# Kernel optimization log

Hardware: AMD Instinct MI355X
Metric: run time of the kernel (lower is better)

## Reference

```python
import jax, jax.numpy as jnp
import numpy as np

HID = 1024   # hidden_size
HEADS = 16   # multi_head
DH = 64      # hidden_size_head
FF = 4096    # ff_size
EPS = 1e-6   # LayerNorm epsilon
NEG = -1e9


def setup_inputs() -> dict:
    key = jax.random.key(0)
    ks = jax.random.split(key, 24)
    B, LI, LQ, LK = 16, 512, 64, 128
    s = 0.02

    def w(k, shape):
        return jax.random.normal(k, shape, jnp.float32) * s

    return {
        "img_feat": jax.random.normal(ks[0], (B, LI, HID), jnp.float32),
        "ques": jax.random.normal(ks[1], (B, LQ, HID), jnp.float32),
        "kg": jax.random.normal(ks[2], (B, LK, HID), jnp.float32),
        "ques_mask": jax.random.randint(ks[3], (B, LQ), 0, 2, jnp.int32),
        "kg_mask": jax.random.randint(ks[4], (B, LK), 0, 2, jnp.int32),
        # stacked params for the 3 MHAtt blocks; torch Linear weight layout [out, in]
        "att_qw": w(ks[5], (3, HID, HID)), "att_qb": jnp.zeros((3, HID), jnp.float32),
        "att_kw": w(ks[6], (3, HID, HID)), "att_kb": jnp.zeros((3, HID), jnp.float32),
        "att_vw": w(ks[7], (3, HID, HID)), "att_vb": jnp.zeros((3, HID), jnp.float32),
        "att_ow": w(ks[8], (3, HID, HID)), "att_ob": jnp.zeros((3, HID), jnp.float32),
        "ffn_w1": w(ks[9], (FF, HID)), "ffn_b1": jnp.zeros((FF,), jnp.float32),
        "ffn_w2": w(ks[10], (HID, FF)), "ffn_b2": jnp.zeros((HID,), jnp.float32),
        "ln_g": jnp.ones((4, HID), jnp.float32), "ln_b": jnp.zeros((4, HID), jnp.float32),
    }


def _ln(x, g, b):
    m = jnp.mean(x, axis=-1, keepdims=True)
    v = jnp.mean(jnp.square(x - m), axis=-1, keepdims=True)
    return g * (x - m) / jnp.sqrt(v + EPS) + b


def _mha(v_in, k_in, q_in, mask, qw, qb, kw, kb, vw, vb, ow, ob):
    B = q_in.shape[0]

    def proj(x, wt, bi):  # [B,S,H] -> [B,heads,S,DH]
        y = jnp.einsum('bsh,oh->bso', x, wt) + bi
        return y.reshape(B, -1, HEADS, DH).transpose(0, 2, 1, 3)

    q = proj(q_in, qw, qb)
    k = proj(k_in, kw, kb)
    v = proj(v_in, vw, vb)
    scores = jnp.einsum('bhqd,bhkd->bhqk', q, k) / jnp.sqrt(jnp.float32(DH))
    if mask is not None:
        scores = jnp.where(mask[:, None, None, :] == 1, NEG, scores)
    a = jax.nn.softmax(scores, axis=-1)  # dropout is identity at eval
    o = jnp.einsum('bhqk,bhkd->bhqd', a, v).transpose(0, 2, 1, 3).reshape(B, -1, HID)
    return jnp.einsum('bsh,oh->bso', o, ow) + ob


def reference(img_feat, ques, kg, ques_mask, kg_mask,
              att_qw, att_qb, att_kw, att_kb, att_vw, att_vb, att_ow, att_ob,
              ffn_w1, ffn_b1, ffn_w2, ffn_b2, ln_g, ln_b):
    x = img_feat
    # self-attention on image features (no mask)
    x = _ln(x + _mha(x, x, x, None,
                     att_qw[0], att_qb[0], att_kw[0], att_kb[0],
                     att_vw[0], att_vb[0], att_ow[0], att_ob[0]), ln_g[0], ln_b[0])
    # cross-attention to question
    x = _ln(x + _mha(ques, ques, x, ques_mask,
                     att_qw[1], att_qb[1], att_kw[1], att_kb[1],
                     att_vw[1], att_vb[1], att_ow[1], att_ob[1]), ln_g[1], ln_b[1])
    # cross-attention to knowledge graph facts
    x = _ln(x + _mha(kg, kg, x, kg_mask,
                     att_qw[2], att_qb[2], att_kw[2], att_kb[2],
                     att_vw[2], att_vb[2], att_ow[2], att_ob[2]), ln_g[2], ln_b[2])
    # FFN: Linear -> ReLU -> Linear (dropout identity at eval)
    h = jax.nn.relu(jnp.einsum('bsh,fh->bsf', x, ffn_w1) + ffn_b1)
    f = jnp.einsum('bsf,hf->bsh', h, ffn_w2) + ffn_b2
    x = _ln(x + f, ln_g[3], ln_b[3])
    return x
```

## Files before the change

kernel.cpp:

```cpp
#include <hip/hip_runtime.h>
#include <math.h>

#define HIDN 1024
#define NHEADS 16
#define DHEAD 64
#define FFD 4096
#define LN_EPS 1e-6f
#define NEGV -1e9f

typedef __bf16 bf16_t;
typedef __bf16 bf16x8 __attribute__((ext_vector_type(8)));
typedef float f32x4 __attribute__((ext_vector_type(4)));
typedef unsigned short ushort8 __attribute__((ext_vector_type(8)));
typedef unsigned short ushort4v __attribute__((ext_vector_type(4)));

__device__ __forceinline__ unsigned short f2bf(float f) {
    unsigned u = __float_as_uint(f);
    return (unsigned short)((u + 0x7FFFu + ((u >> 16) & 1u)) >> 16);
}
__device__ __forceinline__ float bf2f(unsigned short u) {
    return __uint_as_float((unsigned)u << 16);
}
__device__ __forceinline__ void gld16(const void* g, void* l) {
    __builtin_amdgcn_global_load_lds(
        (const __attribute__((address_space(1))) void*)g,
        (__attribute__((address_space(3))) void*)l, 16, 0, 0);
}

template<int RELU>
__global__ __launch_bounds__(256)
void gemm_mfma(const bf16_t* __restrict__ A, const bf16_t* __restrict__ W,
               const float* __restrict__ ba, const float* __restrict__ bb,
               const float* __restrict__ bc, const float* __restrict__ bd,
               unsigned short* __restrict__ Cb, int M, int N, int K)
{
    __shared__ __align__(16) bf16_t As[2][128 * 64];
    __shared__ __align__(16) bf16_t Bs[2][128 * 64];

    const int tid  = threadIdx.x;
    const int wid  = tid >> 6;
    const int lane = tid & 63;
    const int m0 = blockIdx.x * 128;
    const int n0 = blockIdx.y * 128;
    const int wm = (wid & 1) * 64;
    const int wn = (wid >> 1) * 64;

    const int sr = (wid << 3) + (lane >> 3);
    const int sk = (((lane & 7) ^ (lane >> 3)) * 8);
    const bf16_t* pa = A + (size_t)(m0 + sr) * K + sk;
    const bf16_t* pb = W + (size_t)(n0 + sr) * K + sk;
    const int lofs = (wid << 3) * 64;

    const int lr  = lane & 15;
    const int hi_ = lane >> 4;
    const int ch0 = ((hi_ + 0) ^ (lane & 7)) * 8;
    const int ch1 = ((hi_ + 4) ^ (lane & 7)) * 8;

    f32x4 acc[4][4];
    #pragma unroll
    for (int i = 0; i < 4; ++i)
        #pragma unroll
        for (int j = 0; j < 4; ++j) acc[i][j] = (f32x4){0.f, 0.f, 0.f, 0.f};

    auto stage = [&](int buf, int koff) {
        #pragma unroll
        for (int c = 0; c < 4; ++c) {
            gld16(pa + (size_t)c * 32 * K + koff, &As[buf][lofs + c * 32 * 64]);
            gld16(pb + (size_t)c * 32 * K + koff, &Bs[buf][lofs + c * 32 * 64]);
        }
    };
    auto compute = [&](int buf) {
        const bf16_t* fa = &As[buf][(wm + lr) * 64];
        const bf16_t* fb = &Bs[buf][(wn + lr) * 64];
        #pragma unroll
        for (int kk = 0; kk < 2; ++kk) {
            const int ch = kk ? ch1 : ch0;
            bf16x8 a[4], b[4];
            #pragma unroll
            for (int i = 0; i < 4; ++i) {
                a[i] = *(const bf16x8*)(fa + i * 16 * 64 + ch);
                b[i] = *(const bf16x8*)(fb + i * 16 * 64 + ch);
            }
            #pragma unroll
            for (int i = 0; i < 4; ++i)
                #pragma unroll
                for (int j = 0; j < 4; ++j)
                    acc[i][j] = __builtin_amdgcn_mfma_f32_16x16x32_bf16(
                        a[i], b[j], acc[i][j], 0, 0, 0);
        }
    };

    stage(0, 0);
    asm volatile("s_waitcnt vmcnt(0)" ::: "memory");
    __syncthreads();

    for (int k0 = 0; k0 < K; k0 += 128) {
        if (k0 + 64 < K) stage(1, k0 + 64);
        compute(0);
        asm volatile("s_waitcnt vmcnt(0)" ::: "memory");
        __syncthreads();
        if (k0 + 128 < K) stage(0, k0 + 128);
        compute(1);
        asm volatile("s_waitcnt vmcnt(0)" ::: "memory");
        __syncthreads();
    }

    const int seg = n0 >> 10;
    const float* bias = (seg == 0) ? ba : (seg == 1) ? bb : (seg == 2) ? bc : bd;
    const int nl = (n0 & 1023);
    const int er = wm + (lane >> 4) * 4;
    const int ec = wn + (lane & 15);
    float bv[4];
    #pragma unroll
    for (int j = 0; j < 4; ++j) bv[j] = bias[nl + ec + j * 16];
    #pragma unroll
    for (int i = 0; i < 4; ++i)
        #pragma unroll
        for (int j = 0; j < 4; ++j)
            #pragma unroll
            for (int r = 0; r < 4; ++r) {
                float v = acc[i][j][r] + bv[j];
                if (RELU) v = fmaxf(v, 0.f);
                Cb[(size_t)(m0 + er + i * 16 + r) * N + (n0 + ec + j * 16)] = f2bf(v);
            }
}

template<int RELU>
__global__ __launch_bounds__(512, 1)
void gemm_mfma256(const bf16_t* __restrict__ A, const bf16_t* __restrict__ W,
                  const float* __restrict__ ba, const float* __restrict__ bb,
                  const float* __restrict__ bc, const float* __restrict__ bd,
                  unsigned short* __restrict__ Cb, int M, int N, int K)
{
    __shared__ __align__(16) bf16_t As[2][256 * 64];
    __shared__ __align__(16) bf16_t Bs[2][256 * 64];

    const int tid  = threadIdx.x;
    const int wid  = tid >> 6;
    const int lane = tid & 63;
    const int lo   = lane & 15;
    const int hi   = lane >> 4;

    const int GY = gridDim.y;
    const int id = blockIdx.y * gridDim.x + blockIdx.x;
    const int xcd = id & 7;
    const int c   = id >> 3;
    const int CN  = GY >> 1;
    const int m_idx = ((xcd & 3) << 3) + (c & 7);
    const int n_idx = (xcd >> 2) * CN + (c >> 3);
    const int m0 = m_idx * 256;
    const int n0 = n_idx * 256;

    const int wm = (wid & 1) * 128;
    const int wn = (wid >> 1) * 64;

    const int srow = tid >> 3;
    const int ssk  = (((tid & 7) ^ (srow & 7)) * 8);
    const bf16_t* pa = A + (size_t)(m0 + srow) * K + ssk;
    const bf16_t* pb = W + (size_t)(n0 + srow) * K + ssk;
    const int lbase = (wid << 3) * 64;

    auto stage = [&](int buf, int koff) {
        #pragma unroll
        for (int i = 0; i < 4; ++i) {
            gld16(pa + (size_t)i * 64 * K + koff, &As[buf][i * 64 * 64 + lbase]);
            gld16(pb + (size_t)i * 64 * K + koff, &Bs[buf][i * 64 * 64 + lbase]);
        }
    };

    f32x4 acc[8][4];
    #pragma unroll
    for (int f = 0; f < 8; ++f)
        #pragma unroll
        for (int g = 0; g < 4; ++g) acc[f][g] = (f32x4){0.f, 0.f, 0.f, 0.f};

    auto compute = [&](int buf) {
        #pragma unroll
        for (int kk = 0; kk < 2; ++kk) {
            bf16x8 a[8], b[4];
            #pragma unroll
            for (int f = 0; f < 8; ++f) {
                const int row = wm + f * 16 + lo;
                const int ch  = ((kk * 4 + hi) ^ (lo & 7)) * 8;
                a[f] = *(const bf16x8*)&As[buf][row * 64 + ch];
            }
            #pragma unroll
            for (int g = 0; g < 4; ++g) {
                const int row = wn + g * 16 + lo;
                const int ch  = ((kk * 4 + hi) ^ (lo & 7)) * 8;
                b[g] = *(const bf16x8*)&Bs[buf][row * 64 + ch];
            }
            #pragma unroll
            for (int f = 0; f < 8; ++f)
                #pragma unroll
                for (int g = 0; g < 4; ++g)
                    acc[f][g] = __builtin_amdgcn_mfma_f32_16x16x32_bf16(
                        a[f], b[g], acc[f][g], 0, 0, 0);
        }
    };

    stage(0, 0);
    asm volatile("s_waitcnt vmcnt(0)" ::: "memory");
    __syncthreads();

    for (int k0 = 0; k0 < K; k0 += 128) {
        if (k0 + 64 < K) stage(1, k0 + 64);
        compute(0);
        asm volatile("s_waitcnt vmcnt(0)" ::: "memory");
        __syncthreads();
        if (k0 + 128 < K) stage(0, k0 + 128);
        compute(1);
        asm volatile("s_waitcnt vmcnt(0)" ::: "memory");
        __syncthreads();
    }

    const int seg = n0 >> 10;
    const float* bias = (seg == 0) ? ba : (seg == 1) ? bb : (seg == 2) ? bc : bd;
    const int nl = (n0 & 1023);
    float bv[4];
    #pragma unroll
    for (int g = 0; g < 4; ++g) bv[g] = bias[nl + wn + g * 16 + lo];
    #pragma unroll
    for (int f = 0; f < 8; ++f)
        #pragma unroll
        for (int g = 0; g < 4; ++g)
            #pragma unroll
            for (int r = 0; r < 4; ++r) {
                float v = acc[f][g][r] + bv[g];
                if (RELU) v = fmaxf(v, 0.f);
                Cb[(size_t)(m0 + wm + f * 16 + hi * 4 + r) * N
                   + (n0 + wn + g * 16 + lo)] = f2bf(v);
            }
}

template<int HAS_MASK>
__global__ __launch_bounds__(512, 2)
void attn_mfma(const bf16_t* __restrict__ Q, const bf16_t* __restrict__ K,
               const bf16_t* __restrict__ V, int qstride, int kvstride,
               const int* __restrict__ mask,
               unsigned short* __restrict__ O, int Lk)
{
    __shared__ __align__(16) unsigned short Ks[64][72];
    __shared__ __align__(16) unsigned short Vt[64][72];
    __shared__ __align__(16) unsigned short Ps[128][72];
    __shared__ int smask[64];

    const int tid  = threadIdx.x;
    const int wid  = tid >> 6;
    const int lane = tid & 63;
    const int lo   = lane & 15;
    const int hi   = lane >> 4;
    const int h    = blockIdx.x;
    const int b    = blockIdx.y;
    const int Lq   = 512;

    bf16x8 qf[4][2];
    #pragma unroll
    for (int s4 = 0; s4 < 4; ++s4) {
        const bf16_t* qp = Q + (size_t)(b*Lq + s4*128 + wid*16 + lo) * qstride
                             + h*DHEAD + hi*8;
        qf[s4][0] = *(const bf16x8*)qp;
        qf[s4][1] = *(const bf16x8*)(qp + 32);
    }

    float mrun[4][4], lrun[4][4];
    f32x4 Oc[4][4];
    #pragma unroll
    for (int s4 = 0; s4 < 4; ++s4)
        #pragma unroll
        for (int r = 0; r < 4; ++r) {
            mrun[s4][r] = -INFINITY; lrun[s4][r] = 0.f;
            Oc[s4][r] = (f32x4){0.f, 0.f, 0.f, 0.f};
        }

    ushort8 r0, r1;
    int mreg = 0;

    auto load_tile = [&](int k0) {
        if (tid < 256) {
            const int sr = tid >> 2, sc = (tid & 3) * 16;
            const unsigned short* kp = (const unsigned short*)
                (K + (size_t)(b*Lk + k0 + sr) * kvstride + h*DHEAD + sc);
            r0 = *(const ushort8*)kp;
            r1 = *(const ushort8*)(kp + 8);
        } else {
            const int t2 = tid - 256, sr = t2 >> 2, sc = (t2 & 3) * 16;
            const unsigned short* vp = (const unsigned short*)
                (V + (size_t)(b*Lk + k0 + sr) * kvstride + h*DHEAD + sc);
            r0 = *(const ushort8*)vp;
            r1 = *(const ushort8*)(vp + 8);
        }
        if (HAS_MASK && tid < 64) mreg = mask[b*Lk + k0 + tid];
    };
    auto store_tile = [&]() {
        if (tid < 256) {
            const int sr = tid >> 2, sc = (tid & 3) * 16;
            const int x = ((sr >> 3) & 7) << 3;
            *(ushort8*)&Ks[sr][sc ^ x]       = r0;
            *(ushort8*)&Ks[sr][(sc + 8) ^ x] = r1;
        } else {
            const int t2 = tid - 256, sr = t2 >> 2, sc = (t2 & 3) * 16;
            #pragma unroll
            for (int t = 0; t < 8; ++t) {
                const int d0 = sc + t, d1 = sc + 8 + t;
                Vt[d0][sr ^ (((d0 >> 3) & 7) << 3)] = r0[t];
                Vt[d1][sr ^ (((d1 >> 3) & 7) << 3)] = r1[t];
            }
        }
        if (HAS_MASK && tid < 64) smask[tid] = mreg;
    };

    load_tile(0);
    store_tile();
    __syncthreads();

    int k0 = 0;
    while (true) {
        const bool more = (k0 + 64 < Lk);
        if (more) load_tile(k0 + 64);

        #pragma unroll
        for (int s4 = 0; s4 < 4; ++s4) {
            f32x4 sv[4];
            #pragma unroll
            for (int j = 0; j < 4; ++j) sv[j] = (f32x4){0.f, 0.f, 0.f, 0.f};
            #pragma unroll
            for (int kk = 0; kk < 2; ++kk) {
                #pragma unroll
                for (int j = 0; j < 4; ++j) {
                    const int krow = j*16 + lo;
                    const int kcol = (kk*32 + hi*8) ^ (((krow >> 3) & 7) << 3);
                    bf16x8 bfrag = *(const bf16x8*)&Ks[krow][kcol];
                    sv[j] = __builtin_amdgcn_mfma_f32_16x16x32_bf16(
                        qf[s4][kk], bfrag, sv[j], 0, 0, 0);
                }
            }
            #pragma unroll
            for (int j = 0; j < 4; ++j) {
                bool msk = HAS_MASK ? (smask[j*16 + lo] != 0) : false;
                #pragma unroll
                for (int r = 0; r < 4; ++r) {
                    float x = sv[j][r] * 0.125f;
                    sv[j][r] = msk ? NEGV : x;
                }
            }
            #pragma unroll
            for (int r = 0; r < 4; ++r) {
                float tm = fmaxf(fmaxf(sv[0][r], sv[1][r]), fmaxf(sv[2][r], sv[3][r]));
                #pragma unroll
                for (int m = 1; m < 16; m <<= 1) tm = fmaxf(tm, __shfl_xor(tm, m));
                float mnew = fmaxf(mrun[s4][r], tm);
                float f = __expf(mrun[s4][r] - mnew);
                float ps = 0.f;
                #pragma unroll
                for (int j = 0; j < 4; ++j) {
                    float p = __expf(sv[j][r] - mnew);
                    sv[j][r] = p;
                    ps += p;
                }
                #pragma unroll
                for (int m = 1; m < 16; m <<= 1) ps += __shfl_xor(ps, m);
                lrun[s4][r] = lrun[s4][r] * f + ps;
                mrun[s4][r] = mnew;
                #pragma unroll
                for (int n = 0; n < 4; ++n) Oc[s4][n][r] *= f;
                #pragma unroll
                for (int j = 0; j < 4; ++j)
                    Ps[wid*16 + hi*4 + r][j*16 + lo] = f2bf(sv[j][r]);
            }
            #pragma unroll
            for (int kk = 0; kk < 2; ++kk) {
                bf16x8 pa = *(const bf16x8*)&Ps[wid*16 + lo][kk*32 + hi*8];
                #pragma unroll
                for (int n = 0; n < 4; ++n) {
                    const int vrow = n*16 + lo;
                    const int vcol = (kk*32 + hi*8) ^ (((vrow >> 3) & 7) << 3);
                    bf16x8 vf = *(const bf16x8*)&Vt[vrow][vcol];
                    Oc[s4][n] = __builtin_amdgcn_mfma_f32_16x16x32_bf16(
                        pa, vf, Oc[s4][n], 0, 0, 0);
                }
            }
        }

        if (!more) break;
        __syncthreads();
        store_tile();
        __syncthreads();
        k0 += 64;
    }

    #pragma unroll
    for (int s4 = 0; s4 < 4; ++s4)
        #pragma unroll
        for (int r = 0; r < 4; ++r) {
            float inv = 1.f / lrun[s4][r];
            const size_t row = (size_t)(b*Lq + s4*128 + wid*16 + hi*4 + r) * HIDN
                             + h*DHEAD;
            #pragma unroll
            for (int n = 0; n < 4; ++n)
                O[row + n*16 + lo] = f2bf(Oc[s4][n][r] * inv);
        }
}

template<int WF32, int WBF>
__global__ __launch_bounds__(256)
void ln_res_b(const unsigned short* __restrict__ X, const unsigned short* __restrict__ R,
              const float* __restrict__ G, const float* __restrict__ Bv,
              unsigned short* __restrict__ OutB, float* __restrict__ OutF)
{
    const int row = blockIdx.x;
    const int tid = threadIdx.x;
    const size_t base = (size_t)row * HIDN + tid * 4;
    ushort4v xv = *(const ushort4v*)(X + base);
    ushort4v rv = *(const ushort4v*)(R + base);
    float y[4];
    #pragma unroll
    for (int t = 0; t < 4; ++t) y[t] = bf2f(xv[t]) + bf2f(rv[t]);
    float s1 = y[0] + y[1] + y[2] + y[3];
    float s2 = y[0]*y[0] + y[1]*y[1] + y[2]*y[2] + y[3]*y[3];
    #pragma unroll
    for (int m = 1; m < 64; m <<= 1) {
        s1 += __shfl_xor(s1, m);
        s2 += __shfl_xor(s2, m);
    }
    __shared__ float red1[4], red2[4];
    const int wave = tid >> 6, lane = tid & 63;
    if (lane == 0) { red1[wave] = s1; red2[wave] = s2; }
    __syncthreads();
    s1 = red1[0] + red1[1] + red1[2] + red1[3];
    s2 = red2[0] + red2[1] + red2[2] + red2[3];
    const float mean = s1 * (1.f / HIDN);
    const float var  = s2 * (1.f / HIDN) - mean * mean;
    const float inv  = rsqrtf(var + LN_EPS);
    float4 gv = *(const float4*)(G + tid*4);
    float4 bv = *(const float4*)(Bv + tid*4);
    float o[4];
    o[0] = gv.x * (y[0]-mean) * inv + bv.x;
    o[1] = gv.y * (y[1]-mean) * inv + bv.y;
    o[2] = gv.z * (y[2]-mean) * inv + bv.z;
    o[3] = gv.w * (y[3]-mean) * inv + bv.w;
    if (WBF) {
        ushort4v ob;
        #pragma unroll
        for (int t = 0; t < 4; ++t) ob[t] = f2bf(o[t]);
        *(ushort4v*)(OutB + base) = ob;
    }
    if (WF32) {
        float4 of = {o[0], o[1], o[2], o[3]};
        *(float4*)(OutF + base) = of;
    }
}

struct CvtArgs {
    const float* src[32];
    unsigned short* dst[32];
};

__global__ __launch_bounds__(256)
void cvt_units(CvtArgs args)
{
    const float* s = args.src[blockIdx.y];
    unsigned short* d = args.dst[blockIdx.y];
    const int i = blockIdx.x * 256 + threadIdx.x;
    const float4* p = (const float4*)s + (size_t)i * 2;
    float4 a = p[0], b = p[1];
    ushort8 o;
    o[0] = f2bf(a.x); o[1] = f2bf(a.y); o[2] = f2bf(a.z); o[3] = f2bf(a.w);
    o[4] = f2bf(b.x); o[5] = f2bf(b.y); o[6] = f2bf(b.z); o[7] = f2bf(b.w);
    ((ushort8*)d)[i] = o;
}

extern "C" void kernel_launch(void* const* d_in, const int* in_sizes, int n_in,
                              void* d_out, int out_size, void* d_ws, size_t ws_size,
                              hipStream_t stream)
{
    const float* img   = (const float*)d_in[0];
    const float* ques  = (const float*)d_in[1];
    const float* kg    = (const float*)d_in[2];
    const int*   qmask = (const int*)d_in[3];
    const int*   kmask = (const int*)d_in[4];
    const float* qw = (const float*)d_in[5];
    const float* qb = (const float*)d_in[6];
    const float* kw = (const float*)d_in[7];
    const float* kb = (const float*)d_in[8];
    const float* vw = (const float*)d_in[9];
    const float* vb = (const float*)d_in[10];
    const float* ow = (const float*)d_in[11];
    const float* ob = (const float*)d_in[12];
    const float* w1 = (const float*)d_in[13];
    const float* b1 = (const float*)d_in[14];
    const float* w2 = (const float*)d_in[15];
    const float* b2 = (const float*)d_in[16];
    const float* lng = (const float*)d_in[17];
    const float* lnb = (const float*)d_in[18];
    float* out = (float*)d_out;

    const int B = 16;
    const int NX = B * 512;
    const size_t WSTEP = (size_t)1024 * 1024;
    const size_t MB = (size_t)1 << 20;
    const size_t MELEM = (size_t)1024 * 1024;

    char* wsb = (char*)d_ws;
    unsigned short* xb    = (unsigned short*)(wsb);
    unsigned short* bM    = (unsigned short*)(wsb + 16*MB);
    unsigned short* bOb   = (unsigned short*)(wsb + 32*MB);
    unsigned short* quesb = (unsigned short*)(wsb + 48*MB);
    unsigned short* kgb   = (unsigned short*)(wsb + 50*MB);
    unsigned short* wa    = (unsigned short*)(wsb + 56*MB);
    unsigned short* bQKV  = (unsigned short*)(wsb + 96*MB);
    unsigned short* bKV   = (unsigned short*)(wsb + 144*MB);
    unsigned short* hb    = (unsigned short*)(wsb + 96*MB);

    CvtArgs ca;
    int u = 0;
    auto addu = [&](const float* src, int melems, unsigned short* dst) {
        for (int i = 0; i < melems; ++i) {
            ca.src[u] = src + (size_t)i * MELEM;
            ca.dst[u] = dst + (size_t)i * MELEM;
            ++u;
        }
    };
    addu(qw + 0*WSTEP, 1, wa + 0*MELEM);
    addu(kw + 0*WSTEP, 1, wa + 1*MELEM);
    addu(vw + 0*WSTEP, 1, wa + 2*MELEM);
    addu(qw + 1*WSTEP, 1, wa + 3*MELEM);
    addu(kw + 1*WSTEP, 1, wa + 4*MELEM);
    addu(vw + 1*WSTEP, 1, wa + 5*MELEM);
    addu(qw + 2*WSTEP, 1, wa + 6*MELEM);
    addu(kw + 2*WSTEP, 1, wa + 7*MELEM);
    addu(vw + 2*WSTEP, 1, wa + 8*MELEM);
    addu(ow + 0*WSTEP, 1, wa + 9*MELEM);
    addu(ow + 1*WSTEP, 1, wa + 10*MELEM);
    addu(ow + 2*WSTEP, 1, wa + 11*MELEM);
    addu(w1, 4, wa + 12*MELEM);
    addu(w2, 4, wa + 16*MELEM);
    addu(img,  8, xb);
    addu(ques, 1, quesb);
    addu(kg,   2, kgb);

    dim3 blk(256);
    cvt_units<<<dim3(512, u), blk, 0, stream>>>(ca);

    auto gemm = [&](const unsigned short* A, const unsigned short* W,
                    const float* ba, const float* bb_, const float* bc, const float* bd,
                    unsigned short* C, int M, int N, int K, int relu) {
        if (N >= 3072 && (M % 256) == 0 && (N % 256) == 0
            && ((M / 256) % 8) == 0 && ((N / 256) % 2) == 0 && (K % 128) == 0) {
            dim3 grid(M / 256, N / 256);
            if (relu) gemm_mfma256<1><<<grid, dim3(512), 0, stream>>>(
                (const bf16_t*)A, (const bf16_t*)W, ba, bb_, bc, bd, C, M, N, K);
            else      gemm_mfma256<0><<<grid, dim3(512), 0, stream>>>(
                (const bf16_t*)A, (const bf16_t*)W, ba, bb_, bc, bd, C, M, N, K);
            return;
        }
        dim3 grid(M / 128, N / 128);
        if (relu) gemm_mfma<1><<<grid, blk, 0, stream>>>(
            (const bf16_t*)A, (const bf16_t*)W, ba, bb_, bc, bd, C, M, N, K);
        else      gemm_mfma<0><<<grid, blk, 0, stream>>>(
            (const bf16_t*)A, (const bf16_t*)W, ba, bb_, bc, bd, C, M, N, K);
    };

    const unsigned short* Akv[3] = {xb, quesb, kgb};
    const int Mkv[3] = {NX, B * 64, B * 128};
    const int Lk[3]  = {512, 64, 128};

    dim3 ablk(512);
    dim3 agrid(NHEADS, B);

    for (int t = 0; t < 3; ++t) {
        if (t == 0) {
            gemm(xb, wa + 0*MELEM, qb + 0, kb + 0, vb + 0, vb + 0,
                 bQKV, NX, 3072, 1024, 0);
            attn_mfma<0><<<agrid, ablk, 0, stream>>>(
                (const bf16_t*)bQKV, (const bf16_t*)bQKV + 1024, (const bf16_t*)bQKV + 2048,
                3072, 3072, nullptr, bOb, Lk[t]);
        } else {
            gemm(xb, wa + (t == 1 ? 3 : 6)*MELEM,
                 qb + t*1024, qb + t*1024, qb + t*1024, qb + t*1024,
                 bQKV, NX, 1024, 1024, 0);
            gemm(Akv[t], wa + (t == 1 ? 4 : 7)*MELEM,
                 kb + t*1024, vb + t*1024, vb + t*1024, vb + t*1024,
                 bKV, Mkv[t], 2048, 1024, 0);
            attn_mfma<1><<<agrid, ablk, 0, stream>>>(
                (const bf16_t*)bQKV, (const bf16_t*)bKV, (const bf16_t*)bKV + 1024,
                1024, 2048, (t == 1 ? qmask : kmask), bOb, Lk[t]);
        }
        gemm(bOb, wa + (9 + t)*MELEM,
             ob + t*1024, ob + t*1024, ob + t*1024, ob + t*1024,
             bM, NX, 1024, 1024, 0);
        ln_res_b<0,1><<<NX, blk, 0, stream>>>(xb, bM, lng + t*1024, lnb + t*1024, xb, nullptr);
    }

    gemm(xb, wa + 12*MELEM, b1, b1 + 1024, b1 + 2048, b1 + 3072, hb, NX, FFD, 1024, 1);
    gemm(hb, wa + 16*MELEM, b2, b2, b2, b2, bM, NX, 1024, 4096, 0);
    ln_res_b<1,0><<<NX, blk, 0, stream>>>(xb, bM, lng + 3*1024, lnb + 3*1024, nullptr, out);
}
```

Before: 513.5 us.

## Replace double-buffered GEMM staging with 4-slot 32-wide K ring buffer

Restructures the 256x256 MFMA GEMM mainloop from two 64-wide K buffers with a full vmcnt(0) drain each step into a 4-slot ring of 32-wide K slices, kept three stages ahead with partial vmcnt waits and a single barrier per slice. The aim is to keep global-to-LDS loads in flight during compute instead of stalling on every stage. It also raises wave priority around the MFMA block via s_setprio. The cost is more barriers per K and a narrower swizzle (4 chunks per row), which may raise LDS bank conflicts. The dispatch condition is relaxed to K%64.

New measurement: 519.2 us. Within noise of the previous version (+1.1%).

```diff
diff --git a/kernel.cpp b/kernel.cpp
--- a/kernel.cpp
+++ b/kernel.cpp
@@ -132,8 +132,7 @@
                   const float* __restrict__ bc, const float* __restrict__ bd,
                   unsigned short* __restrict__ Cb, int M, int N, int K)
 {
-    __shared__ __align__(16) bf16_t As[2][256 * 64];
-    __shared__ __align__(16) bf16_t Bs[2][256 * 64];
+    __shared__ __align__(16) bf16_t ring[4][2][256 * 32];
 
     const int tid  = threadIdx.x;
     const int wid  = tid >> 6;
@@ -154,19 +153,23 @@
     const int wm = (wid & 1) * 128;
     const int wn = (wid >> 1) * 64;
 
-    const int srow = tid >> 3;
-    const int ssk  = (((tid & 7) ^ (srow & 7)) * 8);
-    const bf16_t* pa = A + (size_t)(m0 + srow) * K + ssk;
-    const bf16_t* pb = W + (size_t)(n0 + srow) * K + ssk;
-    const int lbase = (wid << 3) * 64;
-
-    auto stage = [&](int buf, int koff) {
-        #pragma unroll
-        for (int i = 0; i < 4; ++i) {
-            gld16(pa + (size_t)i * 64 * K + koff, &As[buf][i * 64 * 64 + lbase]);
-            gld16(pb + (size_t)i * 64 * K + koff, &Bs[buf][i * 64 * 64 + lbase]);
-        }
-    };
+    const int srow_in = lane >> 2;
+    const int schunk  = ((lane & 3) ^ (srow_in & 3)) * 8;
+
+    auto stage = [&](int h) {
+        const int s = h & 3;
+        const int koff = (h >> 1) * 64 + (h & 1) * 32;
+        #pragma unroll
+        for (int c16 = 0; c16 < 2; ++c16) {
+            const int row = (wid << 5) + c16 * 16 + srow_in;
+            gld16(A + (size_t)(m0 + row) * K + koff + schunk,
+                  &ring[s][0][((wid << 5) + c16 * 16) * 32]);
+            gld16(W + (size_t)(n0 + row) * K + koff + schunk,
+                  &ring[s][1][((wid << 5) + c16 * 16) * 32]);
+        }
+    };
+
+    const int rch = (hi ^ (lo & 3)) * 8;
 
     f32x4 acc[8][4];
     #pragma unroll
@@ -174,44 +177,37 @@
         #pragma unroll
         for (int g = 0; g < 4; ++g) acc[f][g] = (f32x4){0.f, 0.f, 0.f, 0.f};
 
-    auto compute = [&](int buf) {
-        #pragma unroll
-        for (int kk = 0; kk < 2; ++kk) {
-            bf16x8 a[8], b[4];
-            #pragma unroll
-            for (int f = 0; f < 8; ++f) {
-                const int row = wm + f * 16 + lo;
-                const int ch  = ((kk * 4 + hi) ^ (lo & 7)) * 8;
-                a[f] = *(const bf16x8*)&As[buf][row * 64 + ch];
-            }
-            #pragma unroll
-            for (int g = 0; g < 4; ++g) {
-                const int row = wn + g * 16 + lo;
-                const int ch  = ((kk * 4 + hi) ^ (lo & 7)) * 8;
-                b[g] = *(const bf16x8*)&Bs[buf][row * 64 + ch];
-            }
-            #pragma unroll
-            for (int f = 0; f < 8; ++f)
-                #pragma unroll
-                for (int g = 0; g < 4; ++g)
-                    acc[f][g] = __builtin_amdgcn_mfma_f32_16x16x32_bf16(
-                        a[f], b[g], acc[f][g], 0, 0, 0);
-        }
-    };
-
-    stage(0, 0);
-    asm volatile("s_waitcnt vmcnt(0)" ::: "memory");
-    __syncthreads();
-
-    for (int k0 = 0; k0 < K; k0 += 128) {
-        if (k0 + 64 < K) stage(1, k0 + 64);
-        compute(0);
-        asm volatile("s_waitcnt vmcnt(0)" ::: "memory");
-        __syncthreads();
-        if (k0 + 128 < K) stage(0, k0 + 128);
-        compute(1);
-        asm volatile("s_waitcnt vmcnt(0)" ::: "memory");
-        __syncthreads();
+    auto half_compute = [&](int s) {
+        bf16x8 a[8], b[4];
+        #pragma unroll
+        for (int f = 0; f < 8; ++f)
+            a[f] = *(const bf16x8*)&ring[s][0][(wm + f * 16 + lo) * 32 + rch];
+        #pragma unroll
+        for (int g = 0; g < 4; ++g)
+            b[g] = *(const bf16x8*)&ring[s][1][(wn + g * 16 + lo) * 32 + rch];
+        __builtin_amdgcn_s_setprio(1);
+        #pragma unroll
+        for (int f = 0; f < 8; ++f)
+            #pragma unroll
+            for (int g = 0; g < 4; ++g)
+                acc[f][g] = __builtin_amdgcn_mfma_f32_16x16x32_bf16(
+                    a[f], b[g], acc[f][g], 0, 0, 0);
+        __builtin_amdgcn_s_setprio(0);
+    };
+
+    const int nh = K >> 5;
+
+    stage(0);
+    stage(1);
+    stage(2);
+
+    for (int h = 0; h < nh; ++h) {
+        if (h < nh - 2)      { asm volatile("s_waitcnt vmcnt(8)" ::: "memory"); }
+        else if (h == nh - 2){ asm volatile("s_waitcnt vmcnt(4)" ::: "memory"); }
+        else                 { asm volatile("s_waitcnt vmcnt(0)" ::: "memory"); }
+        __builtin_amdgcn_s_barrier();
+        if (h + 3 < nh) stage(h + 3);
+        half_compute(h & 3);
     }
 
     const int seg = n0 >> 10;
@@ -546,7 +542,8 @@
                     const float* ba, const float* bb_, const float* bc, const float* bd,
                     unsigned short* C, int M, int N, int K, int relu) {
         if (N >= 3072 && (M % 256) == 0 && (N % 256) == 0
-            && ((M / 256) % 8) == 0 && ((N / 256) % 2) == 0 && (K % 128) == 0) {
+            && ((M / 256) % 8) == 0 && ((N / 256) % 2) == 0 && (K % 64) == 0
+            && K >= 128) {
             dim3 grid(M / 256, N / 256);
             if (relu) gemm_mfma256<1><<<grid, dim3(512), 0, stream>>>(
                 (const bf16_t*)A, (const bf16_t*)W, ba, bb_, bc, bd, C, M, N, K);
```
